# Optimization experiments

Measured on AMD Instinct MI355X. Metric: run time of the kernel, lower is better.

## Reference

```python
import jax, jax.numpy as jnp
import numpy as np

N = 16_777_216   # input table length
M = 33_554_432   # number of scatter updates


def setup_inputs() -> dict:
    key = jax.random.key(0)
    k1, k2, k3 = jax.random.split(key, 3)
    input_ = jax.random.randint(k1, (N,), 0, 1000, dtype=jnp.int64)
    index = jax.random.randint(k2, (M,), 0, N, dtype=jnp.int64)
    value = jax.random.randint(k3, (M,), 0, 1000, dtype=jnp.int64)
    return {"input": input_, "index": index, "value": value}


def reference(input, index, value):
    # aten.index_put(input, (index,), value, accumulate=True):
    # out[index[i]] += value[i], duplicates accumulate.
    return input.at[index].add(value)
```

## Files before the change

### kernel.cpp

```cpp
#include <hip/hip_runtime.h>
#include <stdint.h>


#define LOGSLICE  14
#define SLICE     (1 << LOGSLICE)
#define NB        1024
#define CHUNK     8192
#define CNT_THR   256
#define BIN_THR   512
#define EPT       (CHUNK / 4 / BIN_THR)

typedef int  v4i __attribute__((ext_vector_type(4)));
typedef uint32_t v4u __attribute__((ext_vector_type(4)));

#define NTL(x)    __builtin_nontemporal_load(&(x))
#define NTS(p, v) __builtin_nontemporal_store((v), &(p))

__global__ __launch_bounds__(256) void ip_count(const v4i* __restrict__ index4,
                                                uint32_t* __restrict__ gcnt) {
    __shared__ uint32_t cnt[NB];
    const int t = threadIdx.x, c = blockIdx.x;
    for (int i = t; i < NB; i += CNT_THR) cnt[i] = 0;
    __syncthreads();
    const int base4 = c * (CHUNK / 4);
#pragma unroll
    for (int k = 0; k < CHUNK / 4 / CNT_THR; ++k) {
        v4i id = NTL(index4[base4 + t + k * CNT_THR]);
        atomicAdd(&cnt[((uint32_t)id[0]) >> LOGSLICE], 1u);
        atomicAdd(&cnt[((uint32_t)id[1]) >> LOGSLICE], 1u);
        atomicAdd(&cnt[((uint32_t)id[2]) >> LOGSLICE], 1u);
        atomicAdd(&cnt[((uint32_t)id[3]) >> LOGSLICE], 1u);
    }
    __syncthreads();
    for (int i = t; i < NB; i += CNT_THR)
        gcnt[(size_t)c * NB + i] = cnt[i];
}

#define SC_THR  256
#define SC_EPT  16
__global__ __launch_bounds__(256) void ip_scan_chunks(uint32_t* __restrict__ gcnt,
                                                      uint32_t* __restrict__ btotal) {
    __shared__ uint32_t wsum[SC_THR / 64];
    const int t = threadIdx.x;
    const int b = (int)((blockIdx.x & 7) * (gridDim.x >> 3) + (blockIdx.x >> 3));
    const int lane = t & 63, w = t >> 6;

    uint32_t v[SC_EPT];
#pragma unroll
    for (int k = 0; k < SC_EPT; ++k)
        v[k] = gcnt[(size_t)(t * SC_EPT + k) * NB + b];
    uint32_t s = 0;
#pragma unroll
    for (int k = 0; k < SC_EPT; ++k) { uint32_t x = v[k]; v[k] = s; s += x; }

    uint32_t incl = s;
#pragma unroll
    for (int off = 1; off < 64; off <<= 1) {
        uint32_t u = __shfl_up(incl, off);
        if (lane >= off) incl += u;
    }
    if (lane == 63) wsum[w] = incl;
    __syncthreads();
    uint32_t woff = 0;
    for (int i = 0; i < w; ++i) woff += wsum[i];
    const uint32_t base = woff + incl - s;

#pragma unroll
    for (int k = 0; k < SC_EPT; ++k)
        gcnt[(size_t)(t * SC_EPT + k) * NB + b] = base + v[k];

    if (t == SC_THR - 1) btotal[b] = base + s;
}

__global__ __launch_bounds__(1024) void ip_scan_buckets(const uint32_t* __restrict__ btotal,
                                                        uint32_t* __restrict__ bbase) {
    __shared__ uint32_t tmp[NB];
    const int t = threadIdx.x;
    uint32_t v = btotal[t];
    tmp[t] = v; __syncthreads();
    for (int off = 1; off < NB; off <<= 1) {
        uint32_t u = (t >= off) ? tmp[t - off] : 0; __syncthreads();
        tmp[t] += u; __syncthreads();
    }
    bbase[t] = tmp[t] - v;
}

__global__ __launch_bounds__(512) void ip_bin(const v4i* __restrict__ index4,
                                              const v4i* __restrict__ value4,
                                              const uint32_t* __restrict__ gcnt,
                                              const uint32_t* __restrict__ bbase,
                                              uint32_t* __restrict__ pairs) {
    __shared__ uint32_t cur[NB];
    __shared__ uint32_t spk[CHUNK];
    __shared__ uint16_t sbid[CHUNK];
    __shared__ uint32_t wsum[BIN_THR / 64];
    const int t = threadIdx.x;
    const int c = (int)((blockIdx.x & 7) * (gridDim.x >> 3) + (blockIdx.x >> 3));
    const int lane = t & 63, w = t >> 6;

    cur[t * 2 + 0] = 0;
    cur[t * 2 + 1] = 0;
    __syncthreads();

    const int base4 = c * (CHUNK / 4);
    v4i idx[EPT], val[EPT];
#pragma unroll
    for (int k = 0; k < EPT; ++k) {
        idx[k] = NTL(index4[base4 + t + k * BIN_THR]);
        val[k] = NTL(value4[base4 + t + k * BIN_THR]);
    }
    uint32_t lrank[EPT * 4];
#pragma unroll
    for (int k = 0; k < EPT; ++k) {
        lrank[k * 4 + 0] = atomicAdd(&cur[((uint32_t)idx[k][0]) >> LOGSLICE], 1u);
        lrank[k * 4 + 1] = atomicAdd(&cur[((uint32_t)idx[k][1]) >> LOGSLICE], 1u);
        lrank[k * 4 + 2] = atomicAdd(&cur[((uint32_t)idx[k][2]) >> LOGSLICE], 1u);
        lrank[k * 4 + 3] = atomicAdd(&cur[((uint32_t)idx[k][3]) >> LOGSLICE], 1u);
    }
    __syncthreads();

    uint32_t c0 = cur[t * 2 + 0], c1 = cur[t * 2 + 1];
    uint32_t s = c0 + c1;
    uint32_t incl = s;
#pragma unroll
    for (int off = 1; off < 64; off <<= 1) {
        uint32_t u = __shfl_up(incl, off);
        if (lane >= off) incl += u;
    }
    if (lane == 63) wsum[w] = incl;
    __syncthreads();
    uint32_t woff = 0;
    for (int i = 0; i < w; ++i) woff += wsum[i];
    uint32_t ex = woff + incl - s;
    cur[t * 2 + 0] = ex;
    cur[t * 2 + 1] = ex + c0;
    __syncthreads();

#define PLACE(k, cc, e)                                                          \
    {                                                                            \
        uint32_t ix = (uint32_t)idx[k][cc];                                      \
        uint32_t b_ = ix >> LOGSLICE;                                            \
        uint32_t p_ = cur[b_] + lrank[e];                                        \
        spk[p_]  = (((uint32_t)val[k][cc]) << LOGSLICE) | (ix & (SLICE - 1));    \
        sbid[p_] = (uint16_t)b_;                                                 \
    }
#pragma unroll
    for (int k = 0; k < EPT; ++k) {
        PLACE(k, 0, k * 4 + 0) PLACE(k, 1, k * 4 + 1)
        PLACE(k, 2, k * 4 + 2) PLACE(k, 3, k * 4 + 3)
    }
#undef PLACE
    __syncthreads();

#pragma unroll
    for (int r = 0; r < 2; ++r) {
        int i = t + r * BIN_THR;
        cur[i] = bbase[i] + gcnt[(size_t)c * NB + i] - cur[i];
    }
    __syncthreads();

#pragma unroll
    for (int k = 0; k < CHUNK / BIN_THR; ++k) {
        int j = t + k * BIN_THR;
        uint32_t b_ = sbid[j];
        pairs[cur[b_] + (uint32_t)j] = spk[j];
    }
}

__global__ __launch_bounds__(1024) void ip_accumulate(const uint32_t* __restrict__ pairs,
                                                      const uint32_t* __restrict__ btotal,
                                                      const uint32_t* __restrict__ bbase,
                                                      const v4i* __restrict__ input4,
                                                      v4i* __restrict__ out4) {
    __shared__ uint32_t acc[SLICE];
    const int t = threadIdx.x;
    const int b = (int)((blockIdx.x & 7) * (gridDim.x >> 3) + (blockIdx.x >> 3));
    for (int j = t; j < SLICE; j += 1024) acc[j] = 0;
    __syncthreads();

    const uint32_t beg = bbase[b];
    const uint32_t cnt = btotal[b];

    uint32_t head = (4u - (beg & 3u)) & 3u;
    if (head > cnt) head = cnt;
    if (t < (int)head) {
        uint32_t pk = pairs[beg + t];
        atomicAdd(&acc[pk & (SLICE - 1)], pk >> LOGSLICE);
    }
    const uint32_t rem = cnt - head;
    const uint32_t n4  = rem >> 2;
    const uint32_t* __restrict__ p = pairs + beg + head;
    const v4u* __restrict__ p4 = (const v4u*)p;
    for (uint32_t j = t; j < n4; j += 1024) {
        v4u pk = NTL(p4[j]);
        atomicAdd(&acc[pk[0] & (SLICE - 1)], pk[0] >> LOGSLICE);
        atomicAdd(&acc[pk[1] & (SLICE - 1)], pk[1] >> LOGSLICE);
        atomicAdd(&acc[pk[2] & (SLICE - 1)], pk[2] >> LOGSLICE);
        atomicAdd(&acc[pk[3] & (SLICE - 1)], pk[3] >> LOGSLICE);
    }
    for (uint32_t j = (n4 << 2) + t; j < rem; j += 1024) {
        uint32_t pk = p[j];
        atomicAdd(&acc[pk & (SLICE - 1)], pk >> LOGSLICE);
    }
    __syncthreads();

    const int base4 = b * (SLICE / 4);
    for (int j = t; j < SLICE / 4; j += 1024) {
        v4i in = NTL(input4[base4 + j]);
        in[0] += (int)acc[j * 4 + 0];
        in[1] += (int)acc[j * 4 + 1];
        in[2] += (int)acc[j * 4 + 2];
        in[3] += (int)acc[j * 4 + 3];
        NTS(out4[base4 + j], in);
    }
}

__global__ void ip_copy_kernel(const int4* __restrict__ in, int4* __restrict__ out, int n4) {
    int stride = gridDim.x * blockDim.x;
    for (int i = blockIdx.x * blockDim.x + threadIdx.x; i < n4; i += stride)
        out[i] = in[i];
}
__global__ void ip_scatter1_kernel(const int* __restrict__ index, const int* __restrict__ value,
                                   int* __restrict__ out, int m) {
    int stride = gridDim.x * blockDim.x;
    for (int i = blockIdx.x * blockDim.x + threadIdx.x; i < m; i += stride)
        atomicAdd(&out[index[i]], value[i]);
}

extern "C" void kernel_launch(void* const* d_in, const int* in_sizes, int n_in,
                              void* d_out, int out_size, void* d_ws, size_t ws_size,
                              hipStream_t stream) {
    const int* input = (const int*)d_in[0];
    const int* index = (const int*)d_in[1];
    const int* value = (const int*)d_in[2];
    int* out = (int*)d_out;

    const int N = in_sizes[0];
    const int M = in_sizes[1];
    const int B = M / CHUNK;

    const size_t gcnt_bytes = (size_t)B * NB * sizeof(uint32_t);
    const size_t tot_bytes  = NB * sizeof(uint32_t);
    const size_t need = gcnt_bytes + 2 * tot_bytes + (size_t)M * sizeof(uint32_t);

    const bool ok = (N == NB * SLICE) && (M % CHUNK == 0) && (B == SC_THR * SC_EPT) &&
                    (B % 8 == 0) && (ws_size >= need);

    if (ok) {
        uint32_t* gcnt   = (uint32_t*)d_ws;
        uint32_t* btotal = (uint32_t*)((char*)d_ws + gcnt_bytes);
        uint32_t* bbase  = btotal + NB;
        uint32_t* pairs  = bbase + NB;

        ip_count<<<B, CNT_THR, 0, stream>>>((const v4i*)index, gcnt);
        ip_scan_chunks<<<NB, SC_THR, 0, stream>>>(gcnt, btotal);
        ip_scan_buckets<<<1, NB, 0, stream>>>(btotal, bbase);
        ip_bin<<<B, BIN_THR, 0, stream>>>((const v4i*)index, (const v4i*)value,
                                          gcnt, bbase, pairs);
        ip_accumulate<<<NB, 1024, 0, stream>>>(pairs, btotal, bbase,
                                               (const v4i*)input, (v4i*)out);
    } else {
        ip_copy_kernel<<<2048, 256, 0, stream>>>((const int4*)input, (int4*)d_out, N / 4);
        ip_scatter1_kernel<<<2048, 256, 0, stream>>>(index, value, out, M);
    }
}
```

Before: 206.9 us.

## Double binning chunk size and process each chunk in LDS sub-chunks

Doubles the per-block chunk so the per-chunk bucket-count table and its scan get half as many rows. The binning kernel now walks each chunk in four sub-chunks of 4096, carrying running global bucket offsets across them. This keeps the LDS staging buffers small, which should help occupancy. In exchange each block runs more barrier-heavy serial passes, and there are half as many blocks to spread across CUs.

```diff
diff --git a/kernel.cpp b/kernel.cpp
--- a/kernel.cpp
+++ b/kernel.cpp
@@ -5,18 +5,19 @@
 #define LOGSLICE  14
 #define SLICE     (1 << LOGSLICE)
 #define NB        1024
-#define CHUNK     8192
+#define CHUNK     16384
+#define SUB       4096
+#define NSUB      (CHUNK / SUB)
 #define CNT_THR   256
 #define BIN_THR   512
-#define EPT       (CHUNK / 4 / BIN_THR)
-
-typedef int  v4i __attribute__((ext_vector_type(4)));
+
+typedef int      v4i __attribute__((ext_vector_type(4)));
 typedef uint32_t v4u __attribute__((ext_vector_type(4)));
 
 #define NTL(x)    __builtin_nontemporal_load(&(x))
 #define NTS(p, v) __builtin_nontemporal_store((v), &(p))
 
-__global__ __launch_bounds__(256) void ip_count(const v4i* __restrict__ index4,
+__global__ __launch_bounds__(256) void ip_count(const v4u* __restrict__ index4,
                                                 uint32_t* __restrict__ gcnt) {
     __shared__ uint32_t cnt[NB];
     const int t = threadIdx.x, c = blockIdx.x;
@@ -25,11 +26,11 @@
     const int base4 = c * (CHUNK / 4);
 #pragma unroll
     for (int k = 0; k < CHUNK / 4 / CNT_THR; ++k) {
-        v4i id = NTL(index4[base4 + t + k * CNT_THR]);
-        atomicAdd(&cnt[((uint32_t)id[0]) >> LOGSLICE], 1u);
-        atomicAdd(&cnt[((uint32_t)id[1]) >> LOGSLICE], 1u);
-        atomicAdd(&cnt[((uint32_t)id[2]) >> LOGSLICE], 1u);
-        atomicAdd(&cnt[((uint32_t)id[3]) >> LOGSLICE], 1u);
+        v4u id = NTL(index4[base4 + t + k * CNT_THR]);
+        atomicAdd(&cnt[id[0] >> LOGSLICE], 1u);
+        atomicAdd(&cnt[id[1] >> LOGSLICE], 1u);
+        atomicAdd(&cnt[id[2] >> LOGSLICE], 1u);
+        atomicAdd(&cnt[id[3] >> LOGSLICE], 1u);
     }
     __syncthreads();
     for (int i = t; i < NB; i += CNT_THR)
@@ -37,7 +38,7 @@
 }
 
 #define SC_THR  256
-#define SC_EPT  16
+#define SC_EPT  8
 __global__ __launch_bounds__(256) void ip_scan_chunks(uint32_t* __restrict__ gcnt,
                                                       uint32_t* __restrict__ btotal) {
     __shared__ uint32_t wsum[SC_THR / 64];
@@ -85,85 +86,89 @@
     bbase[t] = tmp[t] - v;
 }
 
-__global__ __launch_bounds__(512) void ip_bin(const v4i* __restrict__ index4,
-                                              const v4i* __restrict__ value4,
+__global__ __launch_bounds__(512) void ip_bin(const v4u* __restrict__ index4,
+                                              const v4u* __restrict__ value4,
                                               const uint32_t* __restrict__ gcnt,
                                               const uint32_t* __restrict__ bbase,
                                               uint32_t* __restrict__ pairs) {
-    __shared__ uint32_t cur[NB];
-    __shared__ uint32_t spk[CHUNK];
-    __shared__ uint16_t sbid[CHUNK];
+    __shared__ uint32_t gcur[NB];
+    __shared__ uint32_t lst[NB];
+    __shared__ uint32_t spk[SUB];
+    __shared__ uint16_t sbid[SUB];
     __shared__ uint32_t wsum[BIN_THR / 64];
     const int t = threadIdx.x;
     const int c = (int)((blockIdx.x & 7) * (gridDim.x >> 3) + (blockIdx.x >> 3));
     const int lane = t & 63, w = t >> 6;
 
-    cur[t * 2 + 0] = 0;
-    cur[t * 2 + 1] = 0;
-    __syncthreads();
-
-    const int base4 = c * (CHUNK / 4);
-    v4i idx[EPT], val[EPT];
-#pragma unroll
-    for (int k = 0; k < EPT; ++k) {
-        idx[k] = NTL(index4[base4 + t + k * BIN_THR]);
-        val[k] = NTL(value4[base4 + t + k * BIN_THR]);
-    }
-    uint32_t lrank[EPT * 4];
-#pragma unroll
-    for (int k = 0; k < EPT; ++k) {
-        lrank[k * 4 + 0] = atomicAdd(&cur[((uint32_t)idx[k][0]) >> LOGSLICE], 1u);
-        lrank[k * 4 + 1] = atomicAdd(&cur[((uint32_t)idx[k][1]) >> LOGSLICE], 1u);
-        lrank[k * 4 + 2] = atomicAdd(&cur[((uint32_t)idx[k][2]) >> LOGSLICE], 1u);
-        lrank[k * 4 + 3] = atomicAdd(&cur[((uint32_t)idx[k][3]) >> LOGSLICE], 1u);
-    }
-    __syncthreads();
-
-    uint32_t c0 = cur[t * 2 + 0], c1 = cur[t * 2 + 1];
-    uint32_t s = c0 + c1;
-    uint32_t incl = s;
-#pragma unroll
-    for (int off = 1; off < 64; off <<= 1) {
-        uint32_t u = __shfl_up(incl, off);
-        if (lane >= off) incl += u;
-    }
-    if (lane == 63) wsum[w] = incl;
-    __syncthreads();
-    uint32_t woff = 0;
-    for (int i = 0; i < w; ++i) woff += wsum[i];
-    uint32_t ex = woff + incl - s;
-    cur[t * 2 + 0] = ex;
-    cur[t * 2 + 1] = ex + c0;
-    __syncthreads();
-
-#define PLACE(k, cc, e)                                                          \
-    {                                                                            \
-        uint32_t ix = (uint32_t)idx[k][cc];                                      \
-        uint32_t b_ = ix >> LOGSLICE;                                            \
-        uint32_t p_ = cur[b_] + lrank[e];                                        \
-        spk[p_]  = (((uint32_t)val[k][cc]) << LOGSLICE) | (ix & (SLICE - 1));    \
-        sbid[p_] = (uint16_t)b_;                                                 \
-    }
-#pragma unroll
-    for (int k = 0; k < EPT; ++k) {
-        PLACE(k, 0, k * 4 + 0) PLACE(k, 1, k * 4 + 1)
-        PLACE(k, 2, k * 4 + 2) PLACE(k, 3, k * 4 + 3)
-    }
-#undef PLACE
-    __syncthreads();
-
-#pragma unroll
-    for (int r = 0; r < 2; ++r) {
-        int i = t + r * BIN_THR;
-        cur[i] = bbase[i] + gcnt[(size_t)c * NB + i] - cur[i];
-    }
-    __syncthreads();
-
-#pragma unroll
-    for (int k = 0; k < CHUNK / BIN_THR; ++k) {
-        int j = t + k * BIN_THR;
-        uint32_t b_ = sbid[j];
-        pairs[cur[b_] + (uint32_t)j] = spk[j];
+    gcur[t * 2 + 0] = bbase[t * 2 + 0] + gcnt[(size_t)c * NB + t * 2 + 0];
+    gcur[t * 2 + 1] = bbase[t * 2 + 1] + gcnt[(size_t)c * NB + t * 2 + 1];
+
+    const int cbase4 = c * (CHUNK / 4);
+#pragma unroll 1
+    for (int s = 0; s < NSUB; ++s) {
+        lst[t * 2 + 0] = 0;
+        lst[t * 2 + 1] = 0;
+        __syncthreads();
+
+        v4u idx[2], val[2];
+#pragma unroll
+        for (int k = 0; k < 2; ++k) {
+            idx[k] = NTL(index4[cbase4 + s * (SUB / 4) + t + k * BIN_THR]);
+            val[k] = NTL(value4[cbase4 + s * (SUB / 4) + t + k * BIN_THR]);
+        }
+        uint32_t lrank[8];
+#pragma unroll
+        for (int k = 0; k < 2; ++k) {
+            lrank[k * 4 + 0] = atomicAdd(&lst[idx[k][0] >> LOGSLICE], 1u);
+            lrank[k * 4 + 1] = atomicAdd(&lst[idx[k][1] >> LOGSLICE], 1u);
+            lrank[k * 4 + 2] = atomicAdd(&lst[idx[k][2] >> LOGSLICE], 1u);
+            lrank[k * 4 + 3] = atomicAdd(&lst[idx[k][3] >> LOGSLICE], 1u);
+        }
+        __syncthreads();
+
+        uint32_t c0 = lst[t * 2 + 0], c1 = lst[t * 2 + 1];
+        uint32_t sum = c0 + c1;
+        uint32_t incl = sum;
+#pragma unroll
+        for (int off = 1; off < 64; off <<= 1) {
+            uint32_t u = __shfl_up(incl, off);
+            if (lane >= off) incl += u;
+        }
+        if (lane == 63) wsum[w] = incl;
+        __syncthreads();
+        uint32_t woff = 0;
+        for (int i = 0; i < w; ++i) woff += wsum[i];
+        uint32_t ex = woff + incl - sum;
+        lst[t * 2 + 0] = ex;
+        lst[t * 2 + 1] = ex + c0;
+        __syncthreads();
+
+#pragma unroll
+        for (int k = 0; k < 2; ++k)
+#pragma unroll
+            for (int e = 0; e < 4; ++e) {
+                uint32_t ix = idx[k][e];
+                uint32_t b_ = ix >> LOGSLICE;
+                uint32_t p_ = lst[b_] + lrank[k * 4 + e];
+                spk[p_]  = (val[k][e] << LOGSLICE) | (ix & (SLICE - 1));
+                sbid[p_] = (uint16_t)b_;
+            }
+        __syncthreads();
+
+        lst[t * 2 + 0] = gcur[t * 2 + 0] - lst[t * 2 + 0];
+        lst[t * 2 + 1] = gcur[t * 2 + 1] - lst[t * 2 + 1];
+        __syncthreads();
+
+#pragma unroll
+        for (int k = 0; k < SUB / BIN_THR; ++k) {
+            int j = t + k * BIN_THR;
+            uint32_t b_ = sbid[j];
+            pairs[lst[b_] + (uint32_t)j] = spk[j];
+        }
+        __syncthreads();
+
+        gcur[t * 2 + 0] += c0;
+        gcur[t * 2 + 1] += c1;
     }
 }
 
@@ -252,10 +257,10 @@
         uint32_t* bbase  = btotal + NB;
         uint32_t* pairs  = bbase + NB;
 
-        ip_count<<<B, CNT_THR, 0, stream>>>((const v4i*)index, gcnt);
+        ip_count<<<B, CNT_THR, 0, stream>>>((const v4u*)index, gcnt);
         ip_scan_chunks<<<NB, SC_THR, 0, stream>>>(gcnt, btotal);
         ip_scan_buckets<<<1, NB, 0, stream>>>(btotal, bbase);
-        ip_bin<<<B, BIN_THR, 0, stream>>>((const v4i*)index, (const v4i*)value,
+        ip_bin<<<B, BIN_THR, 0, stream>>>((const v4u*)index, (const v4u*)value,
                                           gcnt, bbase, pairs);
         ip_accumulate<<<NB, 1024, 0, stream>>>(pairs, btotal, bbase,
                                                (const v4i*)input, (v4i*)out);
```

After: 267.6 us. +29.4%, slower.
